# Optimization experiments

Hardware: AMD Instinct MI355X
Metric: run time of the kernel (lower is better)

Reference implementation:

```python
import jax, jax.numpy as jnp
import numpy as np

N = 10000      # nodes
E = 160000     # edges (before self-loops)
IN = 256
NEG_SLOPE = 0.2  # PyG GATConv default


def gat_layer(x, src, dst, W, a_src, a_dst, bias, heads, concat, n):
    # x: [n, in_dim]; W: [in_dim, heads*C]; a_src/a_dst: [heads, C]
    C = W.shape[1] // heads
    h = (x @ W).reshape(n, heads, C)                      # [n,H,C]
    es = jnp.einsum('nhc,hc->nh', h, a_src)               # [n,H]
    ed = jnp.einsum('nhc,hc->nh', h, a_dst)               # [n,H]
    e = jax.nn.leaky_relu(es[src] + ed[dst], NEG_SLOPE)   # [E,H]
    # segment softmax over destination node (every node has a self-loop)
    emax = jax.ops.segment_max(e, dst, num_segments=n)    # [n,H]
    al = jnp.exp(e - emax[dst])                           # [E,H]
    den = jax.ops.segment_sum(al, dst, num_segments=n)    # [n,H]
    al = al / den[dst]
    out = jax.ops.segment_sum(h[src] * al[:, :, None], dst, num_segments=n)  # [n,H,C]
    out = out.reshape(n, heads * C) if concat else out.mean(axis=1)
    return out + bias


def setup_inputs() -> dict:
    key = jax.random.key(0)
    ks = jax.random.split(key, 16)
    s = 0.05
    p = lambda k, shp: jax.random.normal(k, shp, dtype=jnp.float32) * s
    return {
        'x': jax.random.normal(ks[0], (N, IN), dtype=jnp.float32),
        'edge_index': jax.random.randint(ks[1], (2, E), 0, N, dtype=jnp.int64),
        'proj_w': p(ks[2], (IN, 512)), 'proj_b': jnp.zeros((512,), jnp.float32),
        'w1': p(ks[3], (512, 4 * 512)),  'as1': p(ks[4], (4, 512)), 'ad1': p(ks[5], (4, 512)),  'b1': jnp.zeros((2048,), jnp.float32),
        'w2': p(ks[6], (2048, 4 * 512)), 'as2': p(ks[7], (4, 512)), 'ad2': p(ks[8], (4, 512)),  'b2': jnp.zeros((2048,), jnp.float32),
        'w3': p(ks[9], (2048, 2 * 512)), 'as3': p(ks[10], (2, 512)), 'ad3': p(ks[11], (2, 512)), 'b3': jnp.zeros((512,), jnp.float32),
    }


def reference(x, edge_index, proj_w, proj_b, w1, as1, ad1, b1,
              w2, as2, ad2, b2, w3, as3, ad3, b3):
    n = x.shape[0]
    loops = jnp.arange(n, dtype=edge_index.dtype)
    src = jnp.concatenate([edge_index[0], loops])   # PyG add_self_loops=True
    dst = jnp.concatenate([edge_index[1], loops])
    h = x @ proj_w + proj_b                         # dropout is identity in eval
    h = gat_layer(h, src, dst, w1, as1, ad1, b1, 4, True, n)
    h = jax.nn.elu(h)
    h = gat_layer(h, src, dst, w2, as2, ad2, b2, 4, True, n)
    h = jax.nn.elu(h)
    h = gat_layer(h, src, dst, w3, as3, ad3, b3, 2, False, n)
    return h
```

## Files before the change

### kernel.cpp

```cpp
#include <hip/hip_runtime.h>
#include <hip/hip_bf16.h>
#include <math.h>

#define CDIV(a,b) (((a)+(b)-1)/(b))

typedef __bf16  bf16x8 __attribute__((ext_vector_type(8)));
typedef float   f32x4  __attribute__((ext_vector_type(4)));
typedef unsigned short u16x8 __attribute__((ext_vector_type(8)));
typedef unsigned short u16x4 __attribute__((ext_vector_type(4)));

__device__ __forceinline__ float bf2f(unsigned short u) {
    union { unsigned int i; float f; } x; x.i = ((unsigned int)u) << 16; return x.f;
}
__device__ __forceinline__ unsigned short f2bf(float f) {
    union { float f; unsigned int i; } x; x.f = f;
    unsigned int r = x.i + 0x7fff + ((x.i >> 16) & 1);
    return (unsigned short)(r >> 16);
}

__global__ void hist_kernel(const int* __restrict__ ei, int* __restrict__ deg,
                            int E, int Et) {
    int e = blockIdx.x * blockDim.x + threadIdx.x;
    if (e >= Et) return;
    int d = (e < E) ? ei[E + e] : (e - E);
    atomicAdd(&deg[d], 1);
}

__global__ void scan_kernel(const int* __restrict__ deg, int* __restrict__ off, int n) {
    __shared__ int wsum[16];
    __shared__ int carry_s;
    int t = threadIdx.x, lane = t & 63, wv = t >> 6;
    if (t == 0) carry_s = 0;
    __syncthreads();
    for (int base = 0; base < n; base += 1024) {
        int v = (base + t < n) ? deg[base + t] : 0;
        int x = v;
#pragma unroll
        for (int o = 1; o < 64; o <<= 1) {
            int y = __shfl_up(x, o);
            if (lane >= o) x += y;
        }
        if (lane == 63) wsum[wv] = x;
        __syncthreads();
        if (wv == 0 && lane < 16) {
            int s = wsum[lane];
#pragma unroll
            for (int o = 1; o < 16; o <<= 1) {
                int y = __shfl_up(s, o);
                if (lane >= o) s += y;
            }
            wsum[lane] = s;
        }
        __syncthreads();
        int wprev = (wv == 0) ? 0 : wsum[wv - 1];
        int incl = carry_s + wprev + x;
        if (base + t < n) off[base + t] = incl - v;
        __syncthreads();
        if (t == 1023) carry_s = incl;
        __syncthreads();
    }
    if (t == 0) off[n] = carry_s;
}

__global__ void scatter_kernel(const int* __restrict__ ei, const int* __restrict__ off,
                               int* __restrict__ cur, int* __restrict__ csr,
                               int E, int Et) {
    int e = blockIdx.x * blockDim.x + threadIdx.x;
    if (e >= Et) return;
    int s, d;
    if (e < E) { s = ei[e]; d = ei[E + e]; } else { s = e - E; d = s; }
    int pos = off[d] + atomicAdd(&cur[d], 1);
    csr[pos] = s;
}

__global__ void prep_t_kernel(const float* __restrict__ wa, __hip_bfloat16* __restrict__ wta,
                              const float* __restrict__ wb, __hip_bfloat16* __restrict__ wtb,
                              const float* __restrict__ wc, __hip_bfloat16* __restrict__ wtc,
                              int t0, int t1, int t2) {
    __shared__ float tile[32][33];
    int bid = blockIdx.x;
    const float* w; __hip_bfloat16* wt; int K, N, r;
    if (bid < t0)      { w = wa; wt = wta; K = 512;  N = 2048; r = bid; }
    else if (bid < t1) { w = wb; wt = wtb; K = 2048; N = 2048; r = bid - t0; }
    else               { w = wc; wt = wtc; K = 2048; N = 1024; r = bid - t1; }
    (void)t2;
    int kt = K >> 5;
    int kb = (r % kt) * 32, nb = (r / kt) * 32;
    int tx = threadIdx.x & 31, ty = threadIdx.x >> 5;
    for (int i = ty; i < 32; i += 8)
        tile[i][tx] = w[(size_t)(kb + i) * N + nb + tx];
    __syncthreads();
    for (int i = ty; i < 32; i += 8)
        wt[(size_t)(nb + i) * K + kb + tx] = __float2bfloat16(tile[tx][i]);
}

__global__ void cvt2_kernel(const float* __restrict__ a, __hip_bfloat16* __restrict__ ao,
                            int na4,
                            const float* __restrict__ b, __hip_bfloat16* __restrict__ bo,
                            int nb4) {
    int i = blockIdx.x * blockDim.x + threadIdx.x;
    const float* src; __hip_bfloat16* dst; int idx;
    if (i < na4) { src = a; dst = ao; idx = i * 4; }
    else if (i < na4 + nb4) { src = b; dst = bo; idx = (i - na4) * 4; }
    else return;
    float4 v = *(const float4*)(src + idx);
    dst[idx + 0] = __float2bfloat16(v.x);
    dst[idx + 1] = __float2bfloat16(v.y);
    dst[idx + 2] = __float2bfloat16(v.z);
    dst[idx + 3] = __float2bfloat16(v.w);
}

__global__ void beff_kernel(const float* __restrict__ pb, const float* __restrict__ w1,
                            float* __restrict__ beff, int N) {
    int j  = blockIdx.x * 256 + threadIdx.x;
    int k0 = blockIdx.y * 64;
    float s = 0.f;
#pragma unroll
    for (int k = 0; k < 64; k++)
        s = fmaf(pb[k0 + k], w1[(size_t)(k0 + k) * N + j], s);
    atomicAdd(&beff[j], s);
}

__global__ void va_kernel(const __hip_bfloat16* __restrict__ w_efft,
                          const float* __restrict__ b_eff,
                          const float* __restrict__ as1, const float* __restrict__ ad1,
                          const float* __restrict__ b1,
                          float* __restrict__ va, float* __restrict__ cvec,
                          float* __restrict__ b1s) {
    int j = blockIdx.x, t = threadIdx.x;
    if (j == 8) {
        for (int i = t; i < 2048; i += 256) b1s[i] = b_eff[i] + b1[i];
        return;
    }
    int h = j & 3;
    const float* a = ((j < 4) ? as1 : ad1) + h * 512;
    __shared__ float aLDS[512];
    __shared__ float red[256];
    for (int c = t; c < 512; c += 256) aLDS[c] = a[c];
    __syncthreads();
    float acc = 0.f;
    const unsigned short* wb = (const unsigned short*)w_efft + (size_t)h * 512 * 256 + t;
    for (int c = 0; c < 512; c++)
        acc = fmaf(aLDS[c], bf2f(wb[(size_t)c * 256]), acc);
    va[j * 256 + t] = acc;
    float cp = b_eff[h * 512 + t] * aLDS[t] + b_eff[h * 512 + 256 + t] * aLDS[256 + t];
    red[t] = cp;
    __syncthreads();
    for (int s = 128; s > 0; s >>= 1) {
        if (t < s) red[t] += red[t + s];
        __syncthreads();
    }
    if (t == 0) cvec[j] = red[0];
}

__global__ void es1_kernel(const __hip_bfloat16* __restrict__ x_bf,
                           const float* __restrict__ va, const float* __restrict__ cvec,
                           float* __restrict__ es, float* __restrict__ ed) {
    int node = blockIdx.x, l = threadIdx.x;
    u16x4 xv = *(const u16x4*)((const unsigned short*)x_bf + (size_t)node * 256 + l * 4);
    float xf[4];
#pragma unroll
    for (int k = 0; k < 4; k++) xf[k] = bf2f(xv[k]);
    float dot[8];
#pragma unroll
    for (int j = 0; j < 8; j++) {
        float4 v = *(const float4*)(va + j * 256 + l * 4);
        dot[j] = xf[0] * v.x + xf[1] * v.y + xf[2] * v.z + xf[3] * v.w;
    }
#pragma unroll
    for (int j = 0; j < 8; j++)
        for (int o = 32; o; o >>= 1) dot[j] += __shfl_down(dot[j], o);
    if (l == 0) {
#pragma unroll
        for (int h = 0; h < 4; h++) {
            es[node * 4 + h] = dot[h] + cvec[h];
            ed[node * 4 + h] = dot[4 + h] + cvec[4 + h];
        }
    }
}

__global__ __launch_bounds__(256) void agg1x_kernel(
    const __hip_bfloat16* __restrict__ x_bf, const float* __restrict__ es,
    const float* __restrict__ ed, const int* __restrict__ csr,
    const int* __restrict__ off, __hip_bfloat16* __restrict__ z)
{
    __shared__ float alds[64][4];
    __shared__ int   slds[64];
    int d = blockIdx.x, t = threadIdx.x;
    int beg = off[d], end = off[d + 1];
    float acc[4] = {0.f, 0.f, 0.f, 0.f}, den[4] = {0.f, 0.f, 0.f, 0.f};
    float edd[4];
#pragma unroll
    for (int h = 0; h < 4; h++) edd[h] = ed[d * 4 + h];
    const unsigned short* xb = (const unsigned short*)x_bf;

    for (int cb = beg; cb < end; cb += 64) {
        int cl = end - cb; if (cl > 64) cl = 64;
        int i = t >> 2, h = t & 3;
        if (i < cl) {
            int s = csr[cb + i];
            if (h == 0) slds[i] = s;
            float e = es[s * 4 + h] + edd[h];
            e = (e > 0.f) ? e : 0.2f * e;
            alds[i][h] = __expf(e);
        }
        __syncthreads();
        for (int ii = 0; ii < cl; ii++) {
            int s = slds[ii];
            float xv = bf2f(xb[(size_t)s * 256 + t]);
#pragma unroll
            for (int hh = 0; hh < 4; hh++) {
                float a = alds[ii][hh];
                den[hh] += a;
                acc[hh] = fmaf(a, xv, acc[hh]);
            }
        }
        __syncthreads();
    }
    unsigned short* zb = (unsigned short*)z + (size_t)d * 1024;
#pragma unroll
    for (int h = 0; h < 4; h++)
        zb[h * 256 + t] = f2bf(acc[h] / den[h]);
}

__device__ __forceinline__ void gload16(void* lds, const void* g) {
    __builtin_amdgcn_global_load_lds(
        (const __attribute__((address_space(1))) void*)g,
        (__attribute__((address_space(3))) void*)lds, 16, 0, 0);
}

__global__ __launch_bounds__(256) void gemm_bf16_kernel(
    const __hip_bfloat16* __restrict__ A,
    const __hip_bfloat16* __restrict__ BT,
    const float* __restrict__ bias,
    __hip_bfloat16* __restrict__ Cb,
    int M, int N, int K, int lda, int hko, int do_elu,
    int MB, int NB, int XT, int NBH)
{
    __shared__ __align__(16) __hip_bfloat16 As[128 * 32];
    __shared__ __align__(16) __hip_bfloat16 Bs[128 * 32];

    const int bid  = blockIdx.x;
    const int xcd  = bid & 7;
    const int slot = bid >> 3;
    const int per_yh = XT * NBH;
    const int yh    = slot / per_yh;
    const int rem   = slot - yh * per_yh;
    const int x_sub = rem / NBH;
    const int ys    = rem - x_sub * NBH;
    const int yb    = yh * NBH + ys;
    const int xb    = xcd * XT + x_sub;
    if (xb >= MB || yb >= NB) return;

    const int tid = threadIdx.x;
    const int m0 = xb * 128, n0 = yb * 128;
    const int w = tid >> 6, l = tid & 63;
    const int wm = (w & 1) * 64, wn = (w >> 1) * 64;
    const int lm = l & 15, lq = l >> 4;

    f32x4 acc[4][4] = {};

    const int arow = tid >> 2;
    const int acol = (tid & 3) * 8;
    const __hip_bfloat16* Ag = A + (size_t)(m0 + arow) * lda + acol + (n0 >> 9) * hko;
    const __hip_bfloat16* Bg = BT + (size_t)(n0 + arow) * K + acol;
    char* AsW = (char*)As + (w << 10);
    char* BsW = (char*)Bs + (w << 10);

    for (int k0 = 0; k0 < K; k0 += 32) {
        gload16(AsW,        Ag + k0);
        gload16(AsW + 4096, Ag + (size_t)64 * lda + k0);
        gload16(BsW,        Bg + k0);
        gload16(BsW + 4096, Bg + (size_t)64 * K + k0);
        __syncthreads();
        bf16x8 af[4], bfr[4];
#pragma unroll
        for (int i = 0; i < 4; i++)
            af[i] = *(const bf16x8*)(As + (wm + i * 16 + lm) * 32 + lq * 8);
#pragma unroll
        for (int j = 0; j < 4; j++)
            bfr[j] = *(const bf16x8*)(Bs + (wn + j * 16 + lm) * 32 + lq * 8);
#pragma unroll
        for (int i = 0; i < 4; i++)
#pragma unroll
            for (int j = 0; j < 4; j++)
                acc[i][j] = __builtin_amdgcn_mfma_f32_16x16x32_bf16(
                    af[i], bfr[j], acc[i][j], 0, 0, 0);
        __syncthreads();
    }

#pragma unroll
    for (int i = 0; i < 4; i++) {
        int rb = m0 + wm + i * 16 + lq * 4;
#pragma unroll
        for (int r = 0; r < 4; r++) {
            int row = rb + r;
            if (row >= M) continue;
#pragma unroll
            for (int j = 0; j < 4; j++) {
                int col = n0 + wn + j * 16 + lm;
                float v = acc[i][j][r];
                if (bias) v += bias[col];
                if (do_elu) v = (v > 0.f) ? v : expm1f(v);
                Cb[(size_t)row * N + col] = __float2bfloat16(v);
            }
        }
    }
}

__global__ void esed_kernel(const __hip_bfloat16* __restrict__ h,
                            const float* __restrict__ a_src,
                            const float* __restrict__ a_dst,
                            float* __restrict__ es, float* __restrict__ ed, int H) {
    int nidx = blockIdx.x;
    int t = threadIdx.x;
    int head = t >> 6, lane = t & 63;
    const unsigned short* hp =
        (const unsigned short*)h + (size_t)nidx * H * 512 + head * 512 + lane * 8;
    const float* sp = a_src + head * 512 + lane * 8;
    const float* dp = a_dst + head * 512 + lane * 8;
    u16x8 hv = *(const u16x8*)hp;
    float4 s0 = *(const float4*)sp, s1 = *(const float4*)(sp + 4);
    float4 d0 = *(const float4*)dp, d1 = *(const float4*)(dp + 4);
    float hf[8];
#pragma unroll
    for (int k = 0; k < 8; k++) hf[k] = bf2f(hv[k]);
    float s = hf[0]*s0.x + hf[1]*s0.y + hf[2]*s0.z + hf[3]*s0.w
            + hf[4]*s1.x + hf[5]*s1.y + hf[6]*s1.z + hf[7]*s1.w;
    float d = hf[0]*d0.x + hf[1]*d0.y + hf[2]*d0.z + hf[3]*d0.w
            + hf[4]*d1.x + hf[5]*d1.y + hf[6]*d1.z + hf[7]*d1.w;
    for (int o = 32; o; o >>= 1) { s += __shfl_down(s, o); d += __shfl_down(d, o); }
    if (lane == 0) { es[nidx * H + head] = s; ed[nidx * H + head] = d; }
}

template<int H, int VEC, bool MEAN>
__global__ __launch_bounds__(256) void agg_kernel(
    const __hip_bfloat16* __restrict__ h, const float* __restrict__ es,
    const float* __restrict__ ed, const int* __restrict__ csr,
    const int* __restrict__ off, const float* __restrict__ bias,
    float* __restrict__ outF, __hip_bfloat16* __restrict__ outB, int do_elu)
{
    constexpr int HS = H * 512;
    __shared__ float red[MEAN ? 1024 : 1];
    int d = blockIdx.x, t = threadIdx.x;
    int c0 = t * VEC;
    int head = c0 >> 9;
    float edd = ed[d * H + head];
    int beg = off[d], end = off[d + 1];
    float acc[VEC];
#pragma unroll
    for (int k = 0; k < VEC; k++) acc[k] = 0.f;
    float den = 0.f;
    const unsigned short* hb = (const unsigned short*)h;

    int i = beg;
    for (; i + 3 < end; i += 4) {
        int   s[4];
        float wgt[4];
#pragma unroll
        for (int u = 0; u < 4; u++) {
            s[u] = csr[i + u];
            float e = es[s[u] * H + head] + edd;
            e = (e > 0.f) ? e : 0.2f * e;
            wgt[u] = __expf(e);
        }
        if constexpr (VEC == 8) {
            u16x8 v[4];
#pragma unroll
            for (int u = 0; u < 4; u++)
                v[u] = *(const u16x8*)(hb + (size_t)s[u] * HS + c0);
#pragma unroll
            for (int u = 0; u < 4; u++) {
                den += wgt[u];
#pragma unroll
                for (int k = 0; k < 8; k++) acc[k] = fmaf(wgt[u], bf2f(v[u][k]), acc[k]);
            }
        } else {
            u16x4 v[4];
#pragma unroll
            for (int u = 0; u < 4; u++)
                v[u] = *(const u16x4*)(hb + (size_t)s[u] * HS + c0);
#pragma unroll
            for (int u = 0; u < 4; u++) {
                den += wgt[u];
#pragma unroll
                for (int k = 0; k < VEC; k++) acc[k] = fmaf(wgt[u], bf2f(v[u][k]), acc[k]);
            }
        }
    }
    for (; i < end; i++) {
        int s0 = csr[i];
        float e0 = es[s0 * H + head] + edd;
        e0 = (e0 > 0.f) ? e0 : 0.2f * e0;
        float w0 = __expf(e0);
        den += w0;
        const unsigned short* hp0 = hb + (size_t)s0 * HS + c0;
        if constexpr (VEC == 8) {
            u16x8 v0 = *(const u16x8*)hp0;
#pragma unroll
            for (int k = 0; k < 8; k++) acc[k] = fmaf(w0, bf2f(v0[k]), acc[k]);
        } else {
            u16x4 v0 = *(const u16x4*)hp0;
#pragma unroll
            for (int k = 0; k < VEC; k++) acc[k] = fmaf(w0, bf2f(v0[k]), acc[k]);
        }
    }

    float inv = 1.f / den;
    if constexpr (!MEAN) {
        u16x8 ov;
#pragma unroll
        for (int k = 0; k < VEC; k++) {
            float v = acc[k] * inv + bias[c0 + k];
            if (do_elu) v = (v > 0.f) ? v : expm1f(v);
            ov[k] = f2bf(v);
        }
        *(u16x8*)((unsigned short*)outB + (size_t)d * HS + c0) = ov;
    } else {
#pragma unroll
        for (int k = 0; k < VEC; k++) red[c0 + k] = acc[k] * inv;
        __syncthreads();
        if (t < 128) {
#pragma unroll
            for (int k = 0; k < 4; k++) {
                int c = t * 4 + k;
                outF[(size_t)d * 512 + c] = 0.5f * (red[c] + red[c + 512]) + bias[c];
            }
        }
    }
}

extern "C" void kernel_launch(void* const* d_in, const int* in_sizes, int n_in,
                              void* d_out, int out_size, void* d_ws, size_t ws_size,
                              hipStream_t stream) {
    const float* x      = (const float*)d_in[0];
    const int*   ei     = (const int*)  d_in[1];
    const float* proj_w = (const float*)d_in[2];
    const float* proj_b = (const float*)d_in[3];
    const float* w1  = (const float*)d_in[4];
    const float* as1 = (const float*)d_in[5];
    const float* ad1 = (const float*)d_in[6];
    const float* b1  = (const float*)d_in[7];
    const float* w2  = (const float*)d_in[8];
    const float* as2 = (const float*)d_in[9];
    const float* ad2 = (const float*)d_in[10];
    const float* b2  = (const float*)d_in[11];
    const float* w3  = (const float*)d_in[12];
    const float* as3 = (const float*)d_in[13];
    const float* ad3 = (const float*)d_in[14];
    const float* b3  = (const float*)d_in[15];

    const int n    = in_sizes[0] / 256;
    const int E    = in_sizes[1] / 2;
    const int Et   = E + n;
    const int MB   = CDIV(n, 128);
    const int Mpad = MB * 128;
    const int XT   = CDIV(MB, 8);

    char* p = (char*)d_ws;
    auto carve = [&](size_t bytes) {
        void* r = (void*)p;
        p += (bytes + 255) & ~(size_t)255;
        return r;
    };
    __hip_bfloat16* h_bf    = (__hip_bfloat16*)carve((size_t)Mpad * 2048 * sizeof(__hip_bfloat16));
    __hip_bfloat16* act_bf  = (__hip_bfloat16*)carve((size_t)Mpad * 2048 * sizeof(__hip_bfloat16));
    __hip_bfloat16* x_bf    = (__hip_bfloat16*)carve((size_t)Mpad * 256 * sizeof(__hip_bfloat16));
    __hip_bfloat16* pw_bf   = (__hip_bfloat16*)carve((size_t)256 * 512 * sizeof(__hip_bfloat16));
    __hip_bfloat16* w1t     = (__hip_bfloat16*)carve((size_t)2048 * 512 * sizeof(__hip_bfloat16));
    __hip_bfloat16* w2t     = (__hip_bfloat16*)carve((size_t)2048 * 2048 * sizeof(__hip_bfloat16));
    __hip_bfloat16* w3t     = (__hip_bfloat16*)carve((size_t)1024 * 2048 * sizeof(__hip_bfloat16));
    __hip_bfloat16* w_efft  = (__hip_bfloat16*)carve((size_t)2048 * 256 * sizeof(__hip_bfloat16));
    float* b_eff = (float*)carve((size_t)2048 * sizeof(float));
    float* b1s   = (float*)carve((size_t)2048 * sizeof(float));
    float* va    = (float*)carve((size_t)8 * 256 * sizeof(float));
    float* cvec  = (float*)carve((size_t)8 * sizeof(float));
    float* es  = (float*)carve((size_t)n * 4 * sizeof(float));
    float* ed  = (float*)carve((size_t)n * 4 * sizeof(float));
    int* deg = (int*)carve((size_t)2 * n * sizeof(int));
    int* cur = deg + n;
    int* off = (int*)carve((size_t)(n + 1) * sizeof(int));
    int* csr = (int*)carve((size_t)Et * sizeof(int));
    __hip_bfloat16* z_bf = h_bf;
    (void)ws_size; (void)n_in;

    hipMemsetAsync(deg, 0, 2 * n * sizeof(int), stream);
    hipMemsetAsync(b_eff, 0, 2048 * sizeof(float), stream);
    hist_kernel<<<CDIV(Et, 256), 256, 0, stream>>>(ei, deg, E, Et);
    scan_kernel<<<1, 1024, 0, stream>>>(deg, off, n);
    scatter_kernel<<<CDIV(Et, 256), 256, 0, stream>>>(ei, off, cur, csr, E, Et);

    const int t0 = (512 / 32) * (2048 / 32);
    const int t1 = t0 + (2048 / 32) * (2048 / 32);
    const int t2 = t1 + (2048 / 32) * (1024 / 32);
    prep_t_kernel<<<t2, 256, 0, stream>>>(w1, w1t, w2, w2t, w3, w3t, t0, t1, t2);
    const int na4 = 256 * 512 / 4, nb4 = n * 256 / 4;
    cvt2_kernel<<<CDIV(na4 + nb4, 256), 256, 0, stream>>>(proj_w, pw_bf, na4, x, x_bf, nb4);

    gemm_bf16_kernel<<<8 * 2 * 2, 256, 0, stream>>>(
        w1t, pw_bf, nullptr, w_efft, 2048, 256, 512, 512, 0, 0, 16, 2, 2, 2);
    beff_kernel<<<dim3(2048 / 256, 512 / 64), 256, 0, stream>>>(proj_b, w1, b_eff, 2048);

    va_kernel<<<9, 256, 0, stream>>>(w_efft, b_eff, as1, ad1, b1, va, cvec, b1s);

    auto gemm_grid = [&](int NB) { return 8 * XT * NB; };

    es1_kernel<<<n, 64, 0, stream>>>(x_bf, va, cvec, es, ed);
    agg1x_kernel<<<n, 256, 0, stream>>>(x_bf, es, ed, csr, off, z_bf);
    gemm_bf16_kernel<<<gemm_grid(16), 256, 0, stream>>>(
        z_bf, w_efft, b1s, act_bf, n, 2048, 256, 1024, 256, 1, MB, 16, XT, 16);

    gemm_bf16_kernel<<<gemm_grid(16), 256, 0, stream>>>(
        act_bf, w2t, nullptr, h_bf, n, 2048, 2048, 2048, 0, 0, MB, 16, XT, 8);
    esed_kernel<<<n, 4 * 64, 0, stream>>>(h_bf, as2, ad2, es, ed, 4);
    agg_kernel<4, 8, false><<<n, 256, 0, stream>>>(h_bf, es, ed, csr, off, b2,
                                                   nullptr, act_bf, 1);

    gemm_bf16_kernel<<<gemm_grid(8), 256, 0, stream>>>(
        act_bf, w3t, nullptr, h_bf, n, 1024, 2048, 2048, 0, 0, MB, 8, XT, 4);
    esed_kernel<<<n, 2 * 64, 0, stream>>>(h_bf, as3, ad3, es, ed, 2);
    agg_kernel<2, 4, true><<<n, 256, 0, stream>>>(h_bf, es, ed, csr, off, b3,
                                                  (float*)d_out, nullptr, 0);
}
```

Measured before the change: 635.9 us.

## Add 256x256-tile pipelined MFMA GEMM for layer 2 and 3 projections

```diff
diff --git a/kernel.cpp b/kernel.cpp
--- a/kernel.cpp
+++ b/kernel.cpp
@@ -308,6 +308,167 @@
     }
 }
 
+__global__ __launch_bounds__(512, 2) void gemm256_kernel(
+    const __hip_bfloat16* __restrict__ A,
+    const __hip_bfloat16* __restrict__ BT,
+    __hip_bfloat16* __restrict__ Cb,
+    int M, int N, int K, int MT)
+{
+    __shared__ __align__(16) char smem[131072];
+    const int NT = K >> 6;
+
+    const int cpx  = gridDim.x >> 3;
+    const int bid  = blockIdx.x;
+    const int slot = (bid & 7) * cpx + (bid >> 3);
+    const int mt   = slot % MT, ntl = slot / MT;
+    const int m0 = mt << 8, n0 = ntl << 8;
+
+    const int tid = threadIdx.x;
+    const int w  = tid >> 6, l = tid & 63;
+    const int wr = w >> 2, wc = w & 3;
+    const int lm = l & 15, lq = l >> 4;
+
+    const int srow = tid >> 3;
+    const int scol = ((l & 7) << 3) ^ ((l >> 3) << 3);
+    const __hip_bfloat16* As0 = A  + (size_t)(m0 + srow) * K + scol;
+    const __hip_bfloat16* Bs0 = BT + (size_t)(n0 + srow) * K + scol;
+    const size_t rs64  = (size_t)64  * K;
+    const size_t rs128 = (size_t)128 * K;
+    char* const stA = smem +          ((size_t)w << 10);
+    char* const stB = smem + 65536 +  ((size_t)w << 10);
+
+    auto STAGE_A = [&](int par, int hf, int tt) {
+        char* d = stA + (((par << 1) | hf) << 14);
+        const __hip_bfloat16* s = As0 + (size_t)hf * rs128 + (tt << 6);
+        gload16(d,        s);
+        gload16(d + 8192, s + rs64);
+    };
+    auto STAGE_B = [&](int par, int hf, int tt) {
+        char* d = stB + (((par << 1) | hf) << 14);
+        const __hip_bfloat16* s = Bs0 + (size_t)hf * rs128 + (tt << 6);
+        gload16(d,        s);
+        gload16(d + 8192, s + rs64);
+    };
+
+    const int roff = lm << 7;
+    const int xm   = (lm & 7) << 4;
+    const int off0 = (lq << 4) ^ xm;
+    const int off1 = off0 ^ 64;
+    const int bsel = 65536 + ((wc & 1) << 13);
+
+    f32x4  acc[8][4] = {};
+    bf16x8 af[8][2];
+    bf16x8 bfr[2][2];
+
+    STAGE_A(0, 0, 0); STAGE_A(0, 1, 0);
+    STAGE_B(0, 0, 0); STAGE_B(0, 1, 0);
+    STAGE_A(1, 0, 1); STAGE_A(1, 1, 1);
+    asm volatile("s_waitcnt vmcnt(4)" ::: "memory");
+    __builtin_amdgcn_s_barrier();
+
+    for (int t = 0; t < NT; ++t) {
+        const int par = t & 1;
+        const char* aS = smem + (((par << 1) | wr)        << 14) + roff;
+        const char* bS = smem + (((par << 1) | (wc >> 1)) << 14) + bsel + roff;
+
+#pragma unroll
+        for (int i = 0; i < 4; ++i) {
+            af[i][0] = *(const bf16x8*)(aS + i * 2048 + off0);
+            af[i][1] = *(const bf16x8*)(aS + i * 2048 + off1);
+        }
+#pragma unroll
+        for (int j = 0; j < 2; ++j) {
+            bfr[j][0] = *(const bf16x8*)(bS + j * 2048 + off0);
+            bfr[j][1] = *(const bf16x8*)(bS + j * 2048 + off1);
+        }
+        if (t + 1 < NT) STAGE_B(par ^ 1, 0, t + 1);
+        __builtin_amdgcn_s_barrier();
+        asm volatile("s_waitcnt lgkmcnt(0)" ::: "memory");
+        __builtin_amdgcn_sched_barrier(0);
+        __builtin_amdgcn_s_setprio(1);
+#pragma unroll
+        for (int i = 0; i < 4; ++i)
+#pragma unroll
+            for (int j = 0; j < 2; ++j) {
+                acc[i][j] = __builtin_amdgcn_mfma_f32_16x16x32_bf16(af[i][0], bfr[j][0], acc[i][j], 0, 0, 0);
+                acc[i][j] = __builtin_amdgcn_mfma_f32_16x16x32_bf16(af[i][1], bfr[j][1], acc[i][j], 0, 0, 0);
+            }
+        __builtin_amdgcn_s_setprio(0);
+        __builtin_amdgcn_s_barrier();
+
+#pragma unroll
+        for (int i = 4; i < 8; ++i) {
+            af[i][0] = *(const bf16x8*)(aS + i * 2048 + off0);
+            af[i][1] = *(const bf16x8*)(aS + i * 2048 + off1);
+        }
+        if (t + 1 < NT) STAGE_B(par ^ 1, 1, t + 1);
+        __builtin_amdgcn_s_barrier();
+        asm volatile("s_waitcnt lgkmcnt(0)" ::: "memory");
+        __builtin_amdgcn_sched_barrier(0);
+        __builtin_amdgcn_s_setprio(1);
+#pragma unroll
+        for (int i = 4; i < 8; ++i)
+#pragma unroll
+            for (int j = 0; j < 2; ++j) {
+                acc[i][j] = __builtin_amdgcn_mfma_f32_16x16x32_bf16(af[i][0], bfr[j][0], acc[i][j], 0, 0, 0);
+                acc[i][j] = __builtin_amdgcn_mfma_f32_16x16x32_bf16(af[i][1], bfr[j][1], acc[i][j], 0, 0, 0);
+            }
+        __builtin_amdgcn_s_setprio(0);
+        __builtin_amdgcn_s_barrier();
+
+#pragma unroll
+        for (int j = 0; j < 2; ++j) {
+            bfr[j][0] = *(const bf16x8*)(bS + (j + 2) * 2048 + off0);
+            bfr[j][1] = *(const bf16x8*)(bS + (j + 2) * 2048 + off1);
+        }
+        if (t + 2 < NT) STAGE_A(par, 0, t + 2);
+        __builtin_amdgcn_s_barrier();
+        asm volatile("s_waitcnt lgkmcnt(0)" ::: "memory");
+        __builtin_amdgcn_sched_barrier(0);
+        __builtin_amdgcn_s_setprio(1);
+#pragma unroll
+        for (int i = 0; i < 4; ++i)
+#pragma unroll
+            for (int j = 0; j < 2; ++j) {
+                acc[i][j + 2] = __builtin_amdgcn_mfma_f32_16x16x32_bf16(af[i][0], bfr[j][0], acc[i][j + 2], 0, 0, 0);
+                acc[i][j + 2] = __builtin_amdgcn_mfma_f32_16x16x32_bf16(af[i][1], bfr[j][1], acc[i][j + 2], 0, 0, 0);
+            }
+        __builtin_amdgcn_s_setprio(0);
+        __builtin_amdgcn_s_barrier();
+
+        if (t + 2 < NT) STAGE_A(par, 1, t + 2);
+        __builtin_amdgcn_s_barrier();
+        __builtin_amdgcn_sched_barrier(0);
+        __builtin_amdgcn_s_setprio(1);
+#pragma unroll
+        for (int i = 4; i < 8; ++i)
+#pragma unroll
+            for (int j = 0; j < 2; ++j) {
+                acc[i][j + 2] = __builtin_amdgcn_mfma_f32_16x16x32_bf16(af[i][0], bfr[j][0], acc[i][j + 2], 0, 0, 0);
+                acc[i][j + 2] = __builtin_amdgcn_mfma_f32_16x16x32_bf16(af[i][1], bfr[j][1], acc[i][j + 2], 0, 0, 0);
+            }
+        __builtin_amdgcn_s_setprio(0);
+        if (t + 2 < NT)      { asm volatile("s_waitcnt vmcnt(4)" ::: "memory"); }
+        else if (t + 1 < NT) { asm volatile("s_waitcnt vmcnt(0)" ::: "memory"); }
+        __builtin_amdgcn_s_barrier();
+    }
+
+#pragma unroll
+    for (int i = 0; i < 8; ++i) {
+        int rb = m0 + wr * 128 + i * 16 + lq * 4;
+#pragma unroll
+        for (int r = 0; r < 4; ++r) {
+            int row = rb + r;
+            if (row >= M) continue;
+#pragma unroll
+            for (int j = 0; j < 4; ++j) {
+                int col = n0 + wc * 64 + j * 16 + lm;
+                Cb[(size_t)row * N + col] = __float2bfloat16(acc[i][j][r]);
+            }
+        }
+    }
+}
+
 __global__ void esed_kernel(const __hip_bfloat16* __restrict__ h,
                             const float* __restrict__ a_src,
                             const float* __restrict__ a_dst,
@@ -454,7 +615,8 @@
     const int E    = in_sizes[1] / 2;
     const int Et   = E + n;
     const int MB   = CDIV(n, 128);
-    const int Mpad = MB * 128;
+    const int MB2  = CDIV(n, 256);
+    const int Mpad = MB2 * 256;
     const int XT   = CDIV(MB, 8);
 
     char* p = (char*)d_ws;
@@ -510,14 +672,12 @@
     gemm_bf16_kernel<<<gemm_grid(16), 256, 0, stream>>>(
         z_bf, w_efft, b1s, act_bf, n, 2048, 256, 1024, 256, 1, MB, 16, XT, 16);
 
-    gemm_bf16_kernel<<<gemm_grid(16), 256, 0, stream>>>(
-        act_bf, w2t, nullptr, h_bf, n, 2048, 2048, 2048, 0, 0, MB, 16, XT, 8);
+    gemm256_kernel<<<8 * MB2, 512, 0, stream>>>(act_bf, w2t, h_bf, n, 2048, 2048, MB2);
     esed_kernel<<<n, 4 * 64, 0, stream>>>(h_bf, as2, ad2, es, ed, 4);
     agg_kernel<4, 8, false><<<n, 256, 0, stream>>>(h_bf, es, ed, csr, off, b2,
                                                    nullptr, act_bf, 1);
 
-    gemm_bf16_kernel<<<gemm_grid(8), 256, 0, stream>>>(
-        act_bf, w3t, nullptr, h_bf, n, 1024, 2048, 2048, 0, 0, MB, 8, XT, 4);
+    gemm256_kernel<<<4 * MB2, 512, 0, stream>>>(act_bf, w3t, h_bf, n, 1024, 2048, MB2);
     esed_kernel<<<n, 2 * 64, 0, stream>>>(h_bf, as3, ad3, es, ed, 2);
     agg_kernel<2, 4, true><<<n, 256, 0, stream>>>(h_bf, es, ed, csr, off, b3,
                                                   (float*)d_out, nullptr, 0);
```

Result: faster. 619.5 us (-2.6%).
